# Optimization experiments

Measured on AMD Instinct MI355X. Metric: run time of the kernel, lower is better.

The kernel has to match this reference:

```python
import jax, jax.numpy as jnp
import numpy as np

NEG_INF = -1e30

def dwconv1(x, dw, db, pw, pb):
    # DWConv with kernel_size=1: depthwise = per-channel scale+bias, pointwise = dense linear.
    # x: [B, L, H]
    return (x * dw + db) @ pw.T + pb

def masked_softmax(logits, maskf, axis):
    # masked_softmax as in SQuAD repos: mask*logits + (1-mask)*(-1e30), then softmax over axis
    m = maskf * logits + (1.0 - maskf) * NEG_INF
    return jax.nn.softmax(m, axis=axis)

def setup_inputs() -> dict:
    key = jax.random.key(0)
    ks = jax.random.split(key, 20)
    B, L, H = 4, 4096, 1024
    s = 1.0 / np.sqrt(H)
    inp = {
        "x": jax.random.normal(ks[0], (B, L, H), dtype=jnp.float32),
        "mask": jax.random.randint(ks[1], (B, L), 0, 2, dtype=jnp.int32),
    }
    names = ["k", "q", "v", "r"]
    for i, n in enumerate(names):
        inp[n + "_dw"] = jax.random.normal(ks[2 + 4 * i], (H,), dtype=jnp.float32) * 0.1 + 1.0
        inp[n + "_db"] = jnp.zeros((H,), dtype=jnp.float32)
        inp[n + "_pw"] = jax.random.normal(ks[3 + 4 * i], (H, H), dtype=jnp.float32) * s
        inp[n + "_pb"] = jnp.zeros((H,), dtype=jnp.float32)
    return inp

def reference(x, mask, k_dw, k_db, k_pw, k_pb, q_dw, q_db, q_pw, q_pb,
              v_dw, v_db, v_pw, v_pb, r_dw, r_db, r_pw, r_pb):
    B, L, H = x.shape
    n_head = 16
    hc = H // n_head
    maskf = mask.astype(x.dtype)[:, None, None, :]  # [B,1,1,L]

    def heads(t):  # [B,L,H] -> [B,nh,hc,L]
        return t.reshape(B, L, n_head, hc).transpose(0, 2, 3, 1)

    keys = heads(dwconv1(x, k_dw, k_db, k_pw, k_pb))
    queries = heads(dwconv1(x, q_dw, q_db, q_pw, q_pb))
    values = heads(dwconv1(x, v_dw, v_db, v_pw, v_pb))

    key_sm = masked_softmax(keys, maskf, axis=3)      # softmax over L
    query_sm = masked_softmax(queries, maskf, axis=2)  # softmax over head channels

    # context = key @ value^T : [B,nh,hc,hc]
    context = jnp.einsum("bhcl,bhdl->bhcd", key_sm, values)
    # attended = context^T @ query : [B,nh,hc(value),L]
    attended = jnp.einsum("bhcd,bhcl->bhdl", context, query_sm)

    agg = attended.transpose(0, 3, 1, 2).reshape(B, L, H)  # concat heads, [B,L,H]
    # dropout is identity in eval mode
    return dwconv1(agg, r_dw, r_db, r_pw, r_pb)
```

## Files before the change

### kernel.cpp

```cpp
#include <hip/hip_runtime.h>
#include <stdint.h>

#define H 1024
#define LSEQ 4096
#define NBATCH 4
#define MT (NBATCH*LSEQ)

typedef __attribute__((ext_vector_type(8))) short bf16x8;
typedef __attribute__((ext_vector_type(4))) short s16x4;
typedef __attribute__((ext_vector_type(4))) float f32x4;

static __device__ __forceinline__ unsigned short f2bf(float f){
  union { float f; unsigned u; } v; v.f = f;
  unsigned u = v.u;
  return (unsigned short)((u + 0x7FFFu + ((u >> 16) & 1u)) >> 16);
}
static __device__ __forceinline__ float bf2f(unsigned short h){
  union { unsigned u; float f; } v; v.u = ((unsigned)h) << 16;
  return v.f;
}
static __device__ __forceinline__ void g2l16(const void* g, void* l){
  __builtin_amdgcn_global_load_lds((const __attribute__((address_space(1))) void*)g,
                                   (__attribute__((address_space(3))) void*)l, 16, 0, 0);
}
static __device__ __forceinline__ f32x4 mfma16(bf16x8 a, bf16x8 b, f32x4 c){
  return __builtin_amdgcn_mfma_f32_16x16x32_bf16(a, b, c, 0, 0, 0);
}

struct P4 { const float* pw[4]; const float* dw[4]; const float* db[4]; const float* pb[4]; };

__global__ __launch_bounds__(256) void prepcvt(P4 a, const float* __restrict__ x,
    short* __restrict__ wb, float* __restrict__ bo, short* __restrict__ xb){
  const int bid = blockIdx.x, t = threadIdx.x;
  if (bid < 4096){
    __shared__ float red[256];
    const int p = bid >> 10, j = bid & 1023;
    const float* row = a.pw[p] + (size_t)j * H;
    const float* dwp = a.dw[p];
    const float* dbp = a.db[p];
    float acc = 0.f;
    #pragma unroll
    for (int k = 0; k < 4; ++k){
      int i = k*256 + t;
      float pv = row[i];
      wb[((size_t)p*H + j)*H + i] = (short)f2bf(pv * dwp[i]);
      acc += dbp[i] * pv;
    }
    red[t] = acc; __syncthreads();
    for (int s = 128; s > 0; s >>= 1){
      if (t < s) red[t] += red[t+s];
      __syncthreads();
    }
    if (t == 0) bo[p*H + j] = a.pb[p][j] + red[0];
  } else {
    const size_t base = ((size_t)(bid - 4096) * 4096) + (size_t)t * 16;
    #pragma unroll
    for (int h2 = 0; h2 < 2; ++h2){
      const float4* p = (const float4*)(x + base + h2*8);
      float4 u = p[0], v = p[1];
      bf16x8 o;
      o[0]=(short)f2bf(u.x); o[1]=(short)f2bf(u.y); o[2]=(short)f2bf(u.z); o[3]=(short)f2bf(u.w);
      o[4]=(short)f2bf(v.x); o[5]=(short)f2bf(v.y); o[6]=(short)f2bf(v.z); o[7]=(short)f2bf(v.w);
      *(bf16x8*)(xb + base + h2*8) = o;
    }
  }
}

template<int MODE, int NBLK>
__global__ __launch_bounds__(512, 2) void gemm8(const short* __restrict__ A,
    const short* __restrict__ WBp, const float* __restrict__ bia,
    short* __restrict__ oq, short* __restrict__ okT, short* __restrict__ ovT,
    float* __restrict__ ofin){
  __shared__ __align__(16) short lsm[2][2][256*64];

  const int nwg = NBLK * 64;
  const int cpx = nwg >> 3;
  const int bid = blockIdx.x;
  const int swz = (bid & 7) * cpx + (bid >> 3);
  const int mb = swz / NBLK, nb = swz % NBLK;
  const int m0 = mb * 256, n0 = nb * 256;

  const int tid  = threadIdx.x;
  const int lane = tid & 63;
  const int w    = tid >> 6;
  const int wm   = w >> 2, wn = w & 3;
  const int q4 = lane >> 4, r16 = lane & 15;
  const int rl = lane >> 3, sl = lane & 7;
  const int srcsw = ((sl ^ rl) << 3);

#define STAGE_A(BUF_, Q_, KB_) \
  g2l16(A + (size_t)(m0 + (Q_)*64 + w*8 + rl)*H + (KB_) + srcsw, \
        &lsm[0][BUF_][((Q_)*64 + w*8)*64])
#define STAGE_B(BUF_, Q_, KB_) \
  g2l16(WBp + (size_t)(n0 + (Q_)*64 + w*8 + rl)*H + (KB_) + srcsw, \
        &lsm[1][BUF_][((Q_)*64 + w*8)*64])
#define RD_A(dst, BUF_, MI8, KK) { const int row_ = wm*128 + (MI8)*16 + r16; \
  dst = *(const bf16x8*)&lsm[0][BUF_][row_*64 + ((((KK)*4+q4) ^ (row_&7))<<3)]; }
#define RD_B(dst, BUF_, NI4, KK) { const int row_ = wn*64 + (NI4)*16 + r16; \
  dst = *(const bf16x8*)&lsm[1][BUF_][row_*64 + ((((KK)*4+q4) ^ (row_&7))<<3)]; }

  f32x4 acc[8][4] = {};
  bf16x8 aF[4][2], bFa[2][2], bFb[2][2];

  STAGE_B(0,0,0); STAGE_B(0,1,0); STAGE_B(0,2,0); STAGE_B(0,3,0);
  STAGE_A(0,0,0); STAGE_A(0,2,0); STAGE_A(0,1,0); STAGE_A(0,3,0);
  asm volatile("s_waitcnt vmcnt(2)" ::: "memory");
  __builtin_amdgcn_s_barrier();

  #pragma unroll 2
  for (int t = 0; t < 16; ++t){
    const int buf = t & 1, sbuf = buf ^ 1;
    const int skb = ((t < 15) ? (t + 1) : 15) << 6;

    #pragma unroll
    for (int mi = 0; mi < 4; ++mi){ RD_A(aF[mi][0], buf, mi, 0); RD_A(aF[mi][1], buf, mi, 1); }
    #pragma unroll
    for (int ni = 0; ni < 2; ++ni){ RD_B(bFa[ni][0], buf, ni, 0); RD_B(bFa[ni][1], buf, ni, 1); }
    #pragma unroll
    for (int ni = 0; ni < 2; ++ni){ RD_B(bFb[ni][0], buf, 2+ni, 0); RD_B(bFb[ni][1], buf, 2+ni, 1); }
    STAGE_B(sbuf, 0, skb); STAGE_B(sbuf, 1, skb);
    STAGE_B(sbuf, 2, skb); STAGE_B(sbuf, 3, skb);
    __builtin_amdgcn_s_setprio(1);
    #pragma unroll
    for (int kk = 0; kk < 2; ++kk)
      #pragma unroll
      for (int mi = 0; mi < 4; ++mi){
        #pragma unroll
        for (int ni = 0; ni < 2; ++ni)
          acc[mi][ni] = mfma16(aF[mi][kk], bFa[ni][kk], acc[mi][ni]);
        #pragma unroll
        for (int ni = 0; ni < 2; ++ni)
          acc[mi][2+ni] = mfma16(aF[mi][kk], bFb[ni][kk], acc[mi][2+ni]);
      }
    __builtin_amdgcn_s_setprio(0);
    asm volatile("s_waitcnt vmcnt(4)" ::: "memory");
    __builtin_amdgcn_s_barrier();

    #pragma unroll
    for (int mi = 0; mi < 4; ++mi){ RD_A(aF[mi][0], buf, 4+mi, 0); RD_A(aF[mi][1], buf, 4+mi, 1); }
    STAGE_A(sbuf, 0, skb); STAGE_A(sbuf, 2, skb);
    STAGE_A(sbuf, 1, skb); STAGE_A(sbuf, 3, skb);
    __builtin_amdgcn_s_setprio(1);
    #pragma unroll
    for (int kk = 0; kk < 2; ++kk)
      #pragma unroll
      for (int mi = 0; mi < 4; ++mi){
        #pragma unroll
        for (int ni = 0; ni < 2; ++ni)
          acc[4+mi][ni] = mfma16(aF[mi][kk], bFa[ni][kk], acc[4+mi][ni]);
        #pragma unroll
        for (int ni = 0; ni < 2; ++ni)
          acc[4+mi][2+ni] = mfma16(aF[mi][kk], bFb[ni][kk], acc[4+mi][2+ni]);
      }
    __builtin_amdgcn_s_setprio(0);
    asm volatile("s_waitcnt vmcnt(2)" ::: "memory");
    __builtin_amdgcn_s_barrier();
  }
#undef STAGE_A
#undef STAGE_B
#undef RD_A
#undef RD_B

  if (MODE == 1){
    #pragma unroll
    for (int ni4 = 0; ni4 < 4; ++ni4){
      const int n = n0 + wn*64 + ni4*16 + r16;
      const float bv = bia[n];
      #pragma unroll
      for (int mi8 = 0; mi8 < 8; ++mi8){
        const int mbse = m0 + wm*128 + mi8*16 + q4*4;
        #pragma unroll
        for (int j = 0; j < 4; ++j)
          ofin[(size_t)(mbse+j)*H + n] = acc[mi8][ni4][j] + bv;
      }
    }
  } else {
    const int p = n0 >> 10;
    if (p == 1){
      #pragma unroll
      for (int ni4 = 0; ni4 < 4; ++ni4){
        const int n = n0 + wn*64 + ni4*16 + r16;
        const float bv = bia[n];
        const int ch = n & 1023;
        #pragma unroll
        for (int mi8 = 0; mi8 < 8; ++mi8){
          const int mbse = m0 + wm*128 + mi8*16 + q4*4;
          #pragma unroll
          for (int j = 0; j < 4; ++j)
            oq[(size_t)(mbse+j)*H + ch] = (short)f2bf(acc[mi8][ni4][j] + bv);
        }
      }
    } else {
      asm volatile("s_waitcnt vmcnt(0)" ::: "memory");
      __syncthreads();
      char* sC = (char*)&lsm[0][0][0];
      #pragma unroll
      for (int ni4 = 0; ni4 < 4; ++ni4){
        const int cr = wn*64 + ni4*16 + r16;
        const float bv = bia[n0 + cr];
        #pragma unroll
        for (int mi8 = 0; mi8 < 8; ++mi8){
          const int s8 = wm*32 + mi8*4 + q4;
          s16x4 v;
          #pragma unroll
          for (int j = 0; j < 4; ++j) v[j] = (short)f2bf(acc[mi8][ni4][j] + bv);
          *(s16x4*)(sC + cr*512 + ((s8 ^ ((cr & 7) << 1)) << 3)) = v;
        }
      }
      __syncthreads();
      short* ot = (p == 0) ? okT : ovT;
      const int ch0 = n0 & 1023, bb = m0 >> 12, lp0 = m0 & 4095;
      const int c = lane & 31;
      #pragma unroll
      for (int it = 0; it < 16; ++it){
        const int cr = it*16 + w*2 + (lane >> 5);
        bf16x8 vv = *(bf16x8*)(sC + cr*512 + ((c ^ (cr & 7)) << 4));
        *(bf16x8*)&ot[((size_t)bb*H + ch0 + cr)*LSEQ + lp0 + c*8] = vv;
      }
    }
  }
}

__global__ __launch_bounds__(512) void ctx_k(const short* __restrict__ kT,
    const short* __restrict__ vT, const int* __restrict__ mask,
    float* __restrict__ ctxP, float* __restrict__ mloc, float* __restrict__ dloc){
  const int lc = blockIdx.x, h = blockIdx.y, b = blockIdx.z;
  __shared__ __align__(16) short lK[2][64*64];
  __shared__ __align__(16) short lV[2][64*64];
  __shared__ float sMx[64];
  __shared__ float sDenP[8][64];
  __shared__ int sMkG[2][64];
  __shared__ float sAcc[64][65];
  const int tid = threadIdx.x, lane = tid & 63, w = tid >> 6;
  const int grp = w >> 2, wg = w & 3, tig = tid & 255;
  const short* kb = kT + (size_t)(b*16 + h)*64*LSEQ;
  const short* vb = vT + (size_t)(b*16 + h)*64*LSEQ;
  const int l0 = lc*1024;

  int mk16[16];
  {
    const int* mp = mask + (size_t)b*LSEQ + l0;
    int4 a0 = *(const int4*)&mp[lane*8];
    int4 a1 = *(const int4*)&mp[lane*8+4];
    int4 a2 = *(const int4*)&mp[512 + lane*8];
    int4 a3 = *(const int4*)&mp[512 + lane*8+4];
    mk16[0]=a0.x; mk16[1]=a0.y; mk16[2]=a0.z; mk16[3]=a0.w;
    mk16[4]=a1.x; mk16[5]=a1.y; mk16[6]=a1.z; mk16[7]=a1.w;
    mk16[8]=a2.x; mk16[9]=a2.y; mk16[10]=a2.z; mk16[11]=a2.w;
    mk16[12]=a3.x; mk16[13]=a3.y; mk16[14]=a3.z; mk16[15]=a3.w;
  }
  #pragma unroll
  for (int c2 = 0; c2 < 8; ++c2){
    const int ch = w*8 + c2;
    const short* rp = kb + (size_t)ch*LSEQ + l0;
    bf16x8 v0 = *(const bf16x8*)&rp[lane*8];
    bf16x8 v1 = *(const bf16x8*)&rp[512 + lane*8];
    float mm = -1e30f;
    #pragma unroll
    for (int e = 0; e < 8; ++e) if (mk16[e])   mm = fmaxf(mm, bf2f((unsigned short)v0[e]));
    #pragma unroll
    for (int e = 0; e < 8; ++e) if (mk16[8+e]) mm = fmaxf(mm, bf2f((unsigned short)v1[e]));
    #pragma unroll
    for (int off = 32; off >= 1; off >>= 1) mm = fmaxf(mm, __shfl_xor(mm, off));
    if (lane == 0) sMx[ch] = mm;
  }

  f32x4 acc[4] = {};
  float dsum = 0.f;
  const int sl = lane & 7, rl = lane >> 3;
  const int lsw = ((sl ^ rl) << 3);
  __syncthreads();
  for (int kc2 = 0; kc2 < 8; ++kc2){
    const int kc = kc2*2 + grp;
    __syncthreads();
    const int lb = l0 + kc*64;
    #pragma unroll
    for (int c = 0; c < 2; ++c){
      const int r = (wg*2+c)*8 + rl;
      g2l16(kb + (size_t)r*LSEQ + lb + lsw, &lK[grp][(wg*2+c)*512]);
      g2l16(vb + (size_t)r*LSEQ + lb + lsw, &lV[grp][(wg*2+c)*512]);
    }
    if (tig < 64) sMkG[grp][tig] = mask[(size_t)b*LSEQ + lb + tig];
    __syncthreads();
    {
      const int row = lane;
      const float mxr = sMx[row];
      #pragma unroll
      for (int k2 = 0; k2 < 2; ++k2){
        const int slog = wg*2 + k2;
        const int sp = slog ^ (row & 7);
        bf16x8 v = *(bf16x8*)&lK[grp][row*64 + (sp<<3)];
        bf16x8 o;
        #pragma unroll
        for (int e=0;e<8;++e){
          const float f = bf2f((unsigned short)v[e]);
          const float we = sMkG[grp][slog*8+e] ? __expf(f - mxr) : 0.0f;
          dsum += we;
          o[e] = (short)f2bf(we);
        }
        *(bf16x8*)&lK[grp][row*64 + (sp<<3)] = o;
      }
    }
    __syncthreads();
    const int q4 = lane >> 4, r16 = lane & 15;
    #pragma unroll
    for (int kk = 0; kk < 2; ++kk){
      const int slog = kk*4 + q4;
      const int rowA = wg*16 + r16;
      bf16x8 a = *(bf16x8*)&lK[grp][rowA*64 + ((slog ^ (rowA & 7))<<3)];
      #pragma unroll
      for (int ni = 0; ni < 4; ++ni){
        const int rowB = ni*16 + r16;
        bf16x8 bv = *(bf16x8*)&lV[grp][rowB*64 + ((slog ^ (rowB & 7))<<3)];
        acc[ni] = mfma16(a, bv, acc[ni]);
      }
    }
  }
  const int q4 = lane >> 4, r16 = lane & 15;
  sDenP[w][lane] = dsum;
  if (grp == 0){
    #pragma unroll
    for (int ni=0;ni<4;++ni){
      const int d = ni*16 + r16;
      #pragma unroll
      for (int j=0;j<4;++j)
        sAcc[wg*16 + q4*4 + j][d] = acc[ni][j];
    }
  }
  __syncthreads();
  if (grp == 1){
    float* op = ctxP + (((size_t)(b*16 + h)*4 + lc) << 12);
    #pragma unroll
    for (int ni=0;ni<4;++ni){
      const int d = ni*16 + r16;
      #pragma unroll
      for (int j=0;j<4;++j){
        const int c = wg*16 + q4*4 + j;
        op[c*64 + d] = acc[ni][j] + sAcc[c][d];
      }
    }
  }
  if (tid < 64){
    const int idx = (((b*16 + h)*4 + lc) << 6) + tid;
    mloc[idx] = sMx[tid];
    float dv = 0.f;
    #pragma unroll
    for (int ww = 0; ww < 8; ++ww) dv += sDenP[ww][tid];
    dloc[idx] = dv;
  }
}

__global__ __launch_bounds__(512) void attd_k(const short* __restrict__ qb,
    const float* __restrict__ ctxP, const float* __restrict__ mloc,
    const float* __restrict__ dloc, const int* __restrict__ mask,
    short* __restrict__ agg){
  const int lcb = blockIdx.x, h = blockIdx.y, b = blockIdx.z;
  __shared__ __align__(16) short lQ[2][64*64];
  __shared__ __align__(16) short lCt[64*64];
  __shared__ float sSc[4][64];
  const int tid = threadIdx.x, lane = tid & 63, w = tid >> 6;
  const int grp = w >> 2, wg = w & 3;
  if (tid < 64){
    const int base = ((b*16 + h) << 8) + tid;
    float m0 = mloc[base], m1 = mloc[base+64], m2 = mloc[base+128], m3 = mloc[base+192];
    float mg = fmaxf(fmaxf(m0,m1), fmaxf(m2,m3));
    float e0 = __expf(m0-mg), e1 = __expf(m1-mg), e2 = __expf(m2-mg), e3 = __expf(m3-mg);
    float den = e0*dloc[base] + e1*dloc[base+64] + e2*dloc[base+128] + e3*dloc[base+192];
    float inv = 1.0f / fmaxf(den, 1e-30f);
    sSc[0][tid] = e0*inv; sSc[1][tid] = e1*inv; sSc[2][tid] = e2*inv; sSc[3][tid] = e3*inv;
  }
  __syncthreads();
  {
    const int d = lane;
    const float* base = ctxP + ((size_t)(b*16 + h)*4 << 12);
    #pragma unroll
    for (int i=0;i<8;++i){
      const int c = w*8 + i;
      const float s = base[c*64+d]*sSc[0][c] + base[4096+c*64+d]*sSc[1][c]
                    + base[8192+c*64+d]*sSc[2][c] + base[12288+c*64+d]*sSc[3][c];
      lCt[d*64 + ((((c>>3) ^ (d&7))<<3) | (c&7))] = (short)f2bf(s);
    }
  }
  const int l0g = b*LSEQ + lcb*1024 + grp*512;
  const int sl = lane & 7, rl = lane >> 3;
  const int lsw = ((sl ^ rl) << 3);
  for (int sc = 0; sc < 8; ++sc){
    __syncthreads();
    #pragma unroll
    for (int c = 0; c < 2; ++c){
      const int r = (wg*2+c)*8 + rl;
      g2l16(qb + (size_t)(l0g + sc*64 + r)*H + h*64 + lsw, &lQ[grp][(wg*2+c)*512]);
    }
    __syncthreads();
    {
      const int row = wg*16 + (lane & 15);
      const int q4 = lane >> 4;
      const int mk = mask[(size_t)l0g + sc*64 + row];
      float vals[16];
      float mxv = -3e38f;
      #pragma unroll
      for (int k2=0;k2<2;++k2){
        const int slog = q4*2 + k2;
        const int sp = slog ^ (row & 7);
        bf16x8 v = *(bf16x8*)&lQ[grp][row*64 + (sp<<3)];
        #pragma unroll
        for (int e=0;e<8;++e){
          const float f = bf2f((unsigned short)v[e]);
          vals[k2*8+e] = f;
          mxv = fmaxf(mxv, f);
        }
      }
      mxv = fmaxf(mxv, __shfl_xor(mxv, 16));
      mxv = fmaxf(mxv, __shfl_xor(mxv, 32));
      float s = 0.f;
      #pragma unroll
      for (int e=0;e<16;++e){ vals[e] = __expf(vals[e]-mxv); s += vals[e]; }
      s += __shfl_xor(s, 16);
      s += __shfl_xor(s, 32);
      const float inv = 1.0f / s;
      #pragma unroll
      for (int k2=0;k2<2;++k2){
        const int slog = q4*2 + k2;
        const int sp = slog ^ (row & 7);
        bf16x8 o;
        #pragma unroll
        for (int e=0;e<8;++e)
          o[e] = (short)f2bf(mk ? vals[k2*8+e]*inv : 0.015625f);
        *(bf16x8*)&lQ[grp][row*64 + (sp<<3)] = o;
      }
    }
    __syncthreads();
    f32x4 acc[4] = {};
    const int q4 = lane >> 4, r16 = lane & 15;
    #pragma unroll
    for (int kk=0;kk<2;++kk){
      const int slog = kk*4 + q4;
      const int rowA = wg*16 + r16;
      bf16x8 a = *(bf16x8*)&lQ[grp][rowA*64 + ((slog ^ (rowA&7))<<3)];
      #pragma unroll
      for (int ni=0;ni<4;++ni){
        const int rowB = ni*16 + r16;
        bf16x8 bv = *(bf16x8*)&lCt[rowB*64 + ((slog ^ (rowB&7))<<3)];
        acc[ni] = mfma16(a, bv, acc[ni]);
      }
    }
    #pragma unroll
    for (int ni=0;ni<4;++ni){
      const int d = ni*16 + r16;
      #pragma unroll
      for (int j=0;j<4;++j){
        const int lrow = wg*16 + q4*4 + j;
        agg[(size_t)(l0g + sc*64 + lrow)*H + h*64 + d] = (short)f2bf(acc[ni][j]);
      }
    }
  }
}

extern "C" void kernel_launch(void* const* d_in, const int* in_sizes, int n_in,
                              void* d_out, int out_size, void* d_ws, size_t ws_size,
                              hipStream_t stream){
  (void)in_sizes; (void)n_in; (void)out_size; (void)ws_size;
  const float* x    = (const float*)d_in[0];
  const int*   mask = (const int*)d_in[1];
  P4 prm;
  for (int p2 = 0; p2 < 4; ++p2){
    prm.dw[p2] = (const float*)d_in[2 + 4*p2];
    prm.db[p2] = (const float*)d_in[3 + 4*p2];
    prm.pw[p2] = (const float*)d_in[4 + 4*p2];
    prm.pb[p2] = (const float*)d_in[5 + 4*p2];
  }
  char* ws = (char*)d_ws;
  short* WB   = (short*)(ws);
  float* BIAS = (float*)(ws + ((size_t)8<<20));
  float* MLOC = (float*)(ws + ((size_t)8<<20) + (1<<16));
  float* DLOC = (float*)(ws + ((size_t)8<<20) + (2<<16));
  short* XB   = (short*)(ws + ((size_t)9<<20));
  short* QB   = (short*)(ws + ((size_t)41<<20));
  short* KT   = (short*)(ws + ((size_t)73<<20));
  short* VT   = (short*)(ws + ((size_t)105<<20));
  float* CTXP = (float*)(ws + ((size_t)137<<20));
  short* AGG  = XB;

  prepcvt<<<8192, 256, 0, stream>>>(prm, x, WB, BIAS, XB);
  gemm8<0,12><<<768, 512, 0, stream>>>(XB, WB, BIAS, QB, KT, VT, nullptr);
  ctx_k<<<dim3(4,16,4), 512, 0, stream>>>(KT, VT, mask, CTXP, MLOC, DLOC);
  attd_k<<<dim3(4,16,4), 512, 0, stream>>>(QB, CTXP, MLOC, DLOC, mask, AGG);
  gemm8<1,4><<<256, 512, 0, stream>>>(AGG, WB + (size_t)3*H*H, BIAS + 3*1024,
                                      nullptr, nullptr, nullptr, (float*)d_out);
}
```

Baseline: 209.6 us.

## Split context reduction over 8 sequence chunks and issue GEMM loads earlier

The ctx_k kernel now splits each (batch, head) sequence into 8 chunks of 512 instead of 4 chunks of 1024, doubling its grid to 512 blocks. attd_k merges 8 partial max/denominator/context sets instead of 4, and the workspace offsets are widened to hold them. Separately, the GEMM main loop now issues all A and B global-to-LDS staging loads at the start of each iteration, before the LDS fragment reads, and waits with vmcnt(8) instead of vmcnt(4), to overlap memory traffic with compute sooner. More chunks raise occupancy for the context stage but add partial-sum traffic and merge work in attd_k.

```diff
diff --git a/kernel.cpp b/kernel.cpp
--- a/kernel.cpp
+++ b/kernel.cpp
@@ -112,14 +112,16 @@
     const int buf = t & 1, sbuf = buf ^ 1;
     const int skb = ((t < 15) ? (t + 1) : 15) << 6;
 
-    #pragma unroll
-    for (int mi = 0; mi < 4; ++mi){ RD_A(aF[mi][0], buf, mi, 0); RD_A(aF[mi][1], buf, mi, 1); }
-    #pragma unroll
-    for (int ni = 0; ni < 2; ++ni){ RD_B(bFa[ni][0], buf, ni, 0); RD_B(bFa[ni][1], buf, ni, 1); }
-    #pragma unroll
-    for (int ni = 0; ni < 2; ++ni){ RD_B(bFb[ni][0], buf, 2+ni, 0); RD_B(bFb[ni][1], buf, 2+ni, 1); }
     STAGE_B(sbuf, 0, skb); STAGE_B(sbuf, 1, skb);
     STAGE_B(sbuf, 2, skb); STAGE_B(sbuf, 3, skb);
+    STAGE_A(sbuf, 0, skb); STAGE_A(sbuf, 2, skb);
+    STAGE_A(sbuf, 1, skb); STAGE_A(sbuf, 3, skb);
+    #pragma unroll
+    for (int mi = 0; mi < 4; ++mi){ RD_A(aF[mi][0], buf, mi, 0); RD_A(aF[mi][1], buf, mi, 1); }
+    #pragma unroll
+    for (int ni = 0; ni < 2; ++ni){ RD_B(bFa[ni][0], buf, ni, 0); RD_B(bFa[ni][1], buf, ni, 1); }
+    #pragma unroll
+    for (int ni = 0; ni < 2; ++ni){ RD_B(bFb[ni][0], buf, 2+ni, 0); RD_B(bFb[ni][1], buf, 2+ni, 1); }
     __builtin_amdgcn_s_setprio(1);
     #pragma unroll
     for (int kk = 0; kk < 2; ++kk)
@@ -133,13 +135,11 @@
           acc[mi][2+ni] = mfma16(aF[mi][kk], bFb[ni][kk], acc[mi][2+ni]);
       }
     __builtin_amdgcn_s_setprio(0);
-    asm volatile("s_waitcnt vmcnt(4)" ::: "memory");
+    asm volatile("s_waitcnt vmcnt(8)" ::: "memory");
     __builtin_amdgcn_s_barrier();
 
     #pragma unroll
     for (int mi = 0; mi < 4; ++mi){ RD_A(aF[mi][0], buf, 4+mi, 0); RD_A(aF[mi][1], buf, 4+mi, 1); }
-    STAGE_A(sbuf, 0, skb); STAGE_A(sbuf, 2, skb);
-    STAGE_A(sbuf, 1, skb); STAGE_A(sbuf, 3, skb);
     __builtin_amdgcn_s_setprio(1);
     #pragma unroll
     for (int kk = 0; kk < 2; ++kk)
@@ -235,31 +235,24 @@
   const int grp = w >> 2, wg = w & 3, tig = tid & 255;
   const short* kb = kT + (size_t)(b*16 + h)*64*LSEQ;
   const short* vb = vT + (size_t)(b*16 + h)*64*LSEQ;
-  const int l0 = lc*1024;
-
-  int mk16[16];
+  const int l0 = lc*512;
+
+  int mk8[8];
   {
     const int* mp = mask + (size_t)b*LSEQ + l0;
     int4 a0 = *(const int4*)&mp[lane*8];
     int4 a1 = *(const int4*)&mp[lane*8+4];
-    int4 a2 = *(const int4*)&mp[512 + lane*8];
-    int4 a3 = *(const int4*)&mp[512 + lane*8+4];
-    mk16[0]=a0.x; mk16[1]=a0.y; mk16[2]=a0.z; mk16[3]=a0.w;
-    mk16[4]=a1.x; mk16[5]=a1.y; mk16[6]=a1.z; mk16[7]=a1.w;
-    mk16[8]=a2.x; mk16[9]=a2.y; mk16[10]=a2.z; mk16[11]=a2.w;
-    mk16[12]=a3.x; mk16[13]=a3.y; mk16[14]=a3.z; mk16[15]=a3.w;
+    mk8[0]=a0.x; mk8[1]=a0.y; mk8[2]=a0.z; mk8[3]=a0.w;
+    mk8[4]=a1.x; mk8[5]=a1.y; mk8[6]=a1.z; mk8[7]=a1.w;
   }
   #pragma unroll
   for (int c2 = 0; c2 < 8; ++c2){
     const int ch = w*8 + c2;
     const short* rp = kb + (size_t)ch*LSEQ + l0;
     bf16x8 v0 = *(const bf16x8*)&rp[lane*8];
-    bf16x8 v1 = *(const bf16x8*)&rp[512 + lane*8];
     float mm = -1e30f;
     #pragma unroll
-    for (int e = 0; e < 8; ++e) if (mk16[e])   mm = fmaxf(mm, bf2f((unsigned short)v0[e]));
-    #pragma unroll
-    for (int e = 0; e < 8; ++e) if (mk16[8+e]) mm = fmaxf(mm, bf2f((unsigned short)v1[e]));
+    for (int e = 0; e < 8; ++e) if (mk8[e]) mm = fmaxf(mm, bf2f((unsigned short)v0[e]));
     #pragma unroll
     for (int off = 32; off >= 1; off >>= 1) mm = fmaxf(mm, __shfl_xor(mm, off));
     if (lane == 0) sMx[ch] = mm;
@@ -270,7 +263,7 @@
   const int sl = lane & 7, rl = lane >> 3;
   const int lsw = ((sl ^ rl) << 3);
   __syncthreads();
-  for (int kc2 = 0; kc2 < 8; ++kc2){
+  for (int kc2 = 0; kc2 < 4; ++kc2){
     const int kc = kc2*2 + grp;
     __syncthreads();
     const int lb = l0 + kc*64;
@@ -329,7 +322,7 @@
   }
   __syncthreads();
   if (grp == 1){
-    float* op = ctxP + (((size_t)(b*16 + h)*4 + lc) << 12);
+    float* op = ctxP + (((size_t)(b*16 + h)*8 + lc) << 12);
     #pragma unroll
     for (int ni=0;ni<4;++ni){
       const int d = ni*16 + r16;
@@ -341,7 +334,7 @@
     }
   }
   if (tid < 64){
-    const int idx = (((b*16 + h)*4 + lc) << 6) + tid;
+    const int idx = (((b*16 + h)*8 + lc) << 6) + tid;
     mloc[idx] = sMx[tid];
     float dv = 0.f;
     #pragma unroll
@@ -357,27 +350,35 @@
   const int lcb = blockIdx.x, h = blockIdx.y, b = blockIdx.z;
   __shared__ __align__(16) short lQ[2][64*64];
   __shared__ __align__(16) short lCt[64*64];
-  __shared__ float sSc[4][64];
+  __shared__ float sSc[8][64];
   const int tid = threadIdx.x, lane = tid & 63, w = tid >> 6;
   const int grp = w >> 2, wg = w & 3;
   if (tid < 64){
-    const int base = ((b*16 + h) << 8) + tid;
-    float m0 = mloc[base], m1 = mloc[base+64], m2 = mloc[base+128], m3 = mloc[base+192];
-    float mg = fmaxf(fmaxf(m0,m1), fmaxf(m2,m3));
-    float e0 = __expf(m0-mg), e1 = __expf(m1-mg), e2 = __expf(m2-mg), e3 = __expf(m3-mg);
-    float den = e0*dloc[base] + e1*dloc[base+64] + e2*dloc[base+128] + e3*dloc[base+192];
+    const int base = ((b*16 + h) << 9) + tid;
+    float m[8], e[8];
+    #pragma unroll
+    for (int i = 0; i < 8; ++i) m[i] = mloc[base + i*64];
+    float mg = m[0];
+    #pragma unroll
+    for (int i = 1; i < 8; ++i) mg = fmaxf(mg, m[i]);
+    float den = 0.f;
+    #pragma unroll
+    for (int i = 0; i < 8; ++i){ e[i] = __expf(m[i]-mg); den += e[i]*dloc[base + i*64]; }
     float inv = 1.0f / fmaxf(den, 1e-30f);
-    sSc[0][tid] = e0*inv; sSc[1][tid] = e1*inv; sSc[2][tid] = e2*inv; sSc[3][tid] = e3*inv;
+    #pragma unroll
+    for (int i = 0; i < 8; ++i) sSc[i][tid] = e[i]*inv;
   }
   __syncthreads();
   {
     const int d = lane;
-    const float* base = ctxP + ((size_t)(b*16 + h)*4 << 12);
+    const float* base = ctxP + ((size_t)(b*16 + h)*8 << 12);
     #pragma unroll
     for (int i=0;i<8;++i){
       const int c = w*8 + i;
-      const float s = base[c*64+d]*sSc[0][c] + base[4096+c*64+d]*sSc[1][c]
-                    + base[8192+c*64+d]*sSc[2][c] + base[12288+c*64+d]*sSc[3][c];
+      float s = 0.f;
+      #pragma unroll
+      for (int ch = 0; ch < 8; ++ch)
+        s += base[ch*4096 + c*64 + d] * sSc[ch][c];
       lCt[d*64 + ((((c>>3) ^ (d&7))<<3) | (c&7))] = (short)f2bf(s);
     }
   }
@@ -472,8 +473,8 @@
   char* ws = (char*)d_ws;
   short* WB   = (short*)(ws);
   float* BIAS = (float*)(ws + ((size_t)8<<20));
-  float* MLOC = (float*)(ws + ((size_t)8<<20) + (1<<16));
-  float* DLOC = (float*)(ws + ((size_t)8<<20) + (2<<16));
+  float* MLOC = (float*)(ws + ((size_t)8<<20) + (256<<10));
+  float* DLOC = (float*)(ws + ((size_t)8<<20) + (512<<10));
   short* XB   = (short*)(ws + ((size_t)9<<20));
   short* QB   = (short*)(ws + ((size_t)41<<20));
   short* KT   = (short*)(ws + ((size_t)73<<20));
@@ -483,7 +484,7 @@
 
   prepcvt<<<8192, 256, 0, stream>>>(prm, x, WB, BIAS, XB);
   gemm8<0,12><<<768, 512, 0, stream>>>(XB, WB, BIAS, QB, KT, VT, nullptr);
-  ctx_k<<<dim3(4,16,4), 512, 0, stream>>>(KT, VT, mask, CTXP, MLOC, DLOC);
+  ctx_k<<<dim3(8,16,4), 512, 0, stream>>>(KT, VT, mask, CTXP, MLOC, DLOC);
   attd_k<<<dim3(4,16,4), 512, 0, stream>>>(QB, CTXP, MLOC, DLOC, mask, AGG);
   gemm8<1,4><<<256, 512, 0, stream>>>(AGG, WB + (size_t)3*H*H, BIAS + 3*1024,
                                       nullptr, nullptr, nullptr, (float*)d_out);
```

After: 211.3 us. Within noise of the previous version (+0.8%).
